# Kernel tuning notes

Hardware: AMD Instinct MI355X
Metric: run time of the kernel (lower is better)

Reference implementation:

```python
import jax, jax.numpy as jnp
import numpy as np

B, S, DIM, H, DH, DEPTH, NCLS = 4, 2048, 128, 8, 128, 2, 10
M = 128          # number of FAVOR+ random features
CHUNK = 128      # chunk size for causal linear attention
INNER = H * DH   # performer-pytorch: dim_head=dim -> inner_dim = heads*dim
FF = 4 * DIM


def layernorm(x, g, b, eps=1e-5):
    mu = jnp.mean(x, axis=-1, keepdims=True)
    var = jnp.mean((x - mu) ** 2, axis=-1, keepdims=True)
    return (x - mu) * jax.lax.rsqrt(var + eps) * g + b


def softmax_kernel(data, proj, is_query, eps=1e-4):
    # FAVOR+ positive softmax-kernel features. data: [B,H,S,DH], proj: [M,DH]
    norm = DH ** -0.25
    ratio = M ** -0.5
    d = data * norm
    dd = jnp.einsum('bhsd,md->bhsm', d, proj)
    diag = 0.5 * jnp.sum(d * d, axis=-1, keepdims=True)
    if is_query:
        stab = jnp.max(dd, axis=-1, keepdims=True)
    else:
        stab = jnp.max(dd, axis=(-2, -1), keepdims=True)
    stab = jax.lax.stop_gradient(stab)
    return ratio * (jnp.exp(dd - diag - stab) + eps)


def causal_linear_attention(qp, kp, v):
    # qp,kp: [B,H,S,M], v: [B,H,S,DH]; chunked prefix-sum causal linear attention
    b, h, s, m = qp.shape
    d = v.shape[-1]
    nc = s // CHUNK
    def to_chunks(t):
        return t.reshape(b, h, nc, CHUNK, -1).transpose(2, 0, 1, 3, 4)
    qc, kc, vc = to_chunks(qp), to_chunks(kp), to_chunks(v)
    tri = jnp.tril(jnp.ones((CHUNK, CHUNK), qp.dtype))
    def step(carry, inp):
        kv_sum, k_sum = carry           # [b,h,m,d], [b,h,m]
        qi, ki, vi = inp                # [b,h,CHUNK,*]
        attn = jnp.einsum('bhim,bhjm->bhij', qi, ki) * tri
        num = jnp.einsum('bhij,bhjd->bhid', attn, vi) \
            + jnp.einsum('bhim,bhmd->bhid', qi, kv_sum)
        den = jnp.sum(attn, axis=-1) + jnp.einsum('bhim,bhm->bhi', qi, k_sum)
        out = num / (den[..., None] + 1e-6)
        kv_sum = kv_sum + jnp.einsum('bhjm,bhjd->bhmd', ki, vi)
        k_sum = k_sum + jnp.sum(ki, axis=2)
        return (kv_sum, k_sum), out
    init = (jnp.zeros((b, h, m, d), qp.dtype), jnp.zeros((b, h, m), qp.dtype))
    _, out = jax.lax.scan(step, init, (qc, kc, vc))
    return out.transpose(1, 2, 0, 3, 4).reshape(b, h, s, d)


def setup_inputs():
    key = jax.random.key(0)
    ks = jax.random.split(key, 12)
    rng = np.random.default_rng(0)
    # sinusoidal positional encoding [S, DIM]
    pe = np.zeros((S, DIM), np.float32)
    pos = np.arange(S)[:, None].astype(np.float32)
    div = np.exp(np.arange(0, DIM, 2).astype(np.float32) * (-np.log(10000.0) / DIM))
    pe[:, 0::2] = np.sin(pos * div)
    pe[:, 1::2] = np.cos(pos * div)
    # orthogonal random feature projections per layer [DEPTH, M, DH]
    proj = np.stack([
        (np.linalg.qr(rng.standard_normal((DH, DH)))[0][:M] * np.sqrt(DH))
        for _ in range(DEPTH)
    ]).astype(np.float32)
    def gn(k, shape, scale):
        return jax.random.normal(k, shape, jnp.float32) * scale
    return {
        'x': gn(ks[0], (B, S, 1), 1.0),
        'lin_w': gn(ks[1], (1, DIM), 1.0),
        'lin_b': jnp.zeros((DIM,), jnp.float32),
        'pe': jnp.asarray(pe),
        'proj': jnp.asarray(proj),
        'ln1_g': jnp.ones((DEPTH, DIM), jnp.float32),
        'ln1_b': jnp.zeros((DEPTH, DIM), jnp.float32),
        'wq': gn(ks[2], (DEPTH, DIM, INNER), DIM ** -0.5),
        'wk': gn(ks[3], (DEPTH, DIM, INNER), DIM ** -0.5),
        'wv': gn(ks[4], (DEPTH, DIM, INNER), DIM ** -0.5),
        'wo': gn(ks[5], (DEPTH, INNER, DIM), INNER ** -0.5),
        'wo_b': jnp.zeros((DEPTH, DIM), jnp.float32),
        'ln2_g': jnp.ones((DEPTH, DIM), jnp.float32),
        'ln2_b': jnp.zeros((DEPTH, DIM), jnp.float32),
        'ff1_w': gn(ks[6], (DEPTH, DIM, FF), DIM ** -0.5),
        'ff1_b': jnp.zeros((DEPTH, FF), jnp.float32),
        'ff2_w': gn(ks[7], (DEPTH, FF, DIM), FF ** -0.5),
        'ff2_b': jnp.zeros((DEPTH, DIM), jnp.float32),
        'fin_w': gn(ks[8], (DIM, NCLS), DIM ** -0.5),
        'fin_b': jnp.zeros((NCLS,), jnp.float32),
    }


def reference(x, lin_w, lin_b, pe, proj, ln1_g, ln1_b, wq, wk, wv, wo, wo_b,
              ln2_g, ln2_b, ff1_w, ff1_b, ff2_w, ff2_b, fin_w, fin_b):
    h = x @ lin_w + lin_b            # [B,S,DIM]
    h = h + pe[None]
    for l in range(DEPTH):
        # --- pre-norm FAVOR+ causal self-attention ---
        y = layernorm(h, ln1_g[l], ln1_b[l])
        def split(t):  # [B,S,INNER] -> [B,H,S,DH]
            return t.reshape(B, S, H, DH).transpose(0, 2, 1, 3)
        q, k, v = split(y @ wq[l]), split(y @ wk[l]), split(y @ wv[l])
        qp = softmax_kernel(q, proj[l], True)
        kp = softmax_kernel(k, proj[l], False)
        o = causal_linear_attention(qp, kp, v)          # [B,H,S,DH]
        o = o.transpose(0, 2, 1, 3).reshape(B, S, INNER)
        h = h + (o @ wo[l] + wo_b[l])
        # --- pre-norm FFN ---
        y = layernorm(h, ln2_g[l], ln2_b[l])
        f = jax.nn.gelu(y @ ff1_w[l] + ff1_b[l]) @ ff2_w[l] + ff2_b[l]
        h = h + f
    pooled = jnp.mean(h, axis=1)     # [B,DIM]
    return pooled @ fin_w + fin_b    # [B,NCLS]
```

## Files before the change

kernel.cpp:

```cpp
#include <hip/hip_runtime.h>
#include <hip/hip_bf16.h>

#define Bb 4
#define Ss 2048
#define DIMc 128
#define Hh 8
#define DHc 128
#define Mf 128
#define CH 128
#define NCc 16
#define INNERc 1024
#define FFc 512

union F4 { float4 v; float f[4]; };
typedef unsigned short u16;

typedef __bf16 bf16x8 __attribute__((ext_vector_type(8)));
typedef float  f32x4  __attribute__((ext_vector_type(4)));

__device__ __forceinline__ unsigned fkey(float f){
  unsigned b = __float_as_uint(f);
  return (b & 0x80000000u) ? ~b : (b | 0x80000000u);
}
__device__ __forceinline__ float funkey(unsigned u){
  unsigned b = (u & 0x80000000u) ? (u & 0x7fffffffu) : ~u;
  return __uint_as_float(b);
}
__device__ __forceinline__ float gelu_f(float x){
  return 0.5f*x*(1.0f + tanhf(0.7978845608028654f*(x + 0.044715f*x*x*x)));
}
__device__ __forceinline__ u16 f2bu(float f){
  unsigned u = __float_as_uint(f);
  return (u16)((u + 0x7fffu + ((u>>16)&1u)) >> 16);
}
__device__ __forceinline__ float b2f(u16 u){
  return __uint_as_float(((unsigned)u)<<16);
}

__device__ __forceinline__ bf16x8 ldfrag(const u16* base, int row, int e){
  int byte = (row*256 + e*2) ^ ((row&7)<<4);
  return *(const bf16x8*)((const char*)base + byte);
}
__device__ __forceinline__ void stage_lin_bf(u16* dst, const u16* src, int srs, int t){
  #pragma unroll
  for(int it=0; it<8; ++it){
    int idx = t + it*256; int r = idx>>4, c8 = idx&15;
    int byte = (r*256 + c8*16) ^ ((r&7)<<4);
    *(uint4*)((char*)dst + byte) = *(const uint4*)(src + r*srs + c8*8);
  }
}
__device__ __forceinline__ void stage_lin_bf_s(u16* dst, const u16* src, int srs,
    int t, float sc, float off){
  #pragma unroll
  for(int it=0; it<8; ++it){
    int idx = t + it*256; int r = idx>>4, c8 = idx&15;
    u16 tmp[8]; *(uint4*)tmp = *(const uint4*)(src + r*srs + c8*8);
    #pragma unroll
    for(int u=0;u<8;u++) tmp[u] = f2bu(fmaf(b2f(tmp[u]), sc, off));
    int byte = (r*256 + c8*16) ^ ((r&7)<<4);
    *(uint4*)((char*)dst + byte) = *(uint4*)tmp;
  }
}
__device__ __forceinline__ void stage_lin_f32(u16* dst, const float* src, int srs, int t){
  #pragma unroll
  for(int it=0; it<8; ++it){
    int idx = t + it*256; int r = idx>>4, c8 = idx&15;
    F4 v0, v1;
    v0.v = *(const float4*)(src + r*srs + c8*8);
    v1.v = *(const float4*)(src + r*srs + c8*8 + 4);
    u16 tmp[8];
    #pragma unroll
    for(int u=0;u<4;u++){ tmp[u] = f2bu(v0.f[u]); tmp[4+u] = f2bu(v1.f[u]); }
    int byte = (r*256 + c8*16) ^ ((r&7)<<4);
    *(uint4*)((char*)dst + byte) = *(uint4*)tmp;
  }
}
__device__ __forceinline__ void stage_tr_bf(u16* dst, const u16* src, int srs, int t){
  int j0 = (t & 63)*2; int wv = t>>6;
  #pragma unroll
  for(int it=0; it<2; ++it){
    int d0 = wv*16 + it*64;
    u16 a0[16], a1[16];
    *(uint4*)&a0[0] = *(const uint4*)(src + j0*srs + d0);
    *(uint4*)&a0[8] = *(const uint4*)(src + j0*srs + d0 + 8);
    *(uint4*)&a1[0] = *(const uint4*)(src + (j0+1)*srs + d0);
    *(uint4*)&a1[8] = *(const uint4*)(src + (j0+1)*srs + d0 + 8);
    #pragma unroll
    for(int dc=0; dc<16; ++dc){
      int d = d0 + dc;
      unsigned pk = (unsigned)a0[dc] | ((unsigned)a1[dc]<<16);
      int byte = (d*256 + j0*2) ^ ((d&7)<<4);
      *(unsigned*)((char*)dst + byte) = pk;
    }
  }
}
__device__ __forceinline__ void stage_tr_bf_s(u16* dst, const u16* src, int srs,
    int t, float sc, float off){
  int j0 = (t & 63)*2; int wv = t>>6;
  #pragma unroll
  for(int it=0; it<2; ++it){
    int d0 = wv*16 + it*64;
    u16 a0[16], a1[16];
    *(uint4*)&a0[0] = *(const uint4*)(src + j0*srs + d0);
    *(uint4*)&a0[8] = *(const uint4*)(src + j0*srs + d0 + 8);
    *(uint4*)&a1[0] = *(const uint4*)(src + (j0+1)*srs + d0);
    *(uint4*)&a1[8] = *(const uint4*)(src + (j0+1)*srs + d0 + 8);
    #pragma unroll
    for(int dc=0; dc<16; ++dc){
      int d = d0 + dc;
      unsigned pk = (unsigned)f2bu(fmaf(b2f(a0[dc]), sc, off)) |
                    ((unsigned)f2bu(fmaf(b2f(a1[dc]), sc, off))<<16);
      int byte = (d*256 + j0*2) ^ ((d&7)<<4);
      *(unsigned*)((char*)dst + byte) = pk;
    }
  }
}

__device__ __forceinline__ int2 swz_tile(){
  int nx = gridDim.x;
  int nwg = gridDim.x*gridDim.y;
  int lin = blockIdx.y*nx + blockIdx.x;
  int q = nwg>>3, r = nwg&7;
  int xcd = lin&7, idx = lin>>3;
  int nl = (xcd<r) ? (xcd*(q+1)+idx) : (r*(q+1)+(xcd-r)*q+idx);
  return make_int2(nl % nx, nl / nx);
}

__global__ __launch_bounds__(64) void k_init(unsigned* kstab){
  if(threadIdx.x < 64) kstab[threadIdx.x] = 0u;
}

__global__ __launch_bounds__(256) void k_embed(const float* __restrict__ x,
    const float* __restrict__ lw, const float* __restrict__ lb,
    const float* __restrict__ pe, float* __restrict__ h){
  int idx = blockIdx.x*256 + threadIdx.x;
  int d = idx & 127; int bs = idx >> 7; int s = bs & (Ss-1);
  h[idx] = x[bs]*lw[d] + lb[d] + pe[s*DIMc + d];
}

__global__ __launch_bounds__(256) void k_ln(const float* __restrict__ in,
    const float* __restrict__ g, const float* __restrict__ bta,
    u16* __restrict__ out){
  int wave = threadIdx.x >> 6; int lane = threadIdx.x & 63;
  int row = blockIdx.x*4 + wave;
  const float* r = in + row*DIMc;
  float x1 = r[lane], x2 = r[lane+64];
  float s = x1+x2, sq = x1*x1 + x2*x2;
  #pragma unroll
  for(int m=1;m<64;m<<=1){ s += __shfl_xor(s,m,64); sq += __shfl_xor(sq,m,64); }
  float mu = s * (1.0f/128.0f);
  float var = sq*(1.0f/128.0f) - mu*mu;
  float rs = rsqrtf(var + 1e-5f);
  out[row*DIMc+lane]    = f2bu((x1-mu)*rs*g[lane]+bta[lane]);
  out[row*DIMc+lane+64] = f2bu((x2-mu)*rs*g[lane+64]+bta[lane+64]);
}

template<bool QKV3, bool BIAS, bool GELU>
__global__ __launch_bounds__(256) void k_gemm128(const u16* __restrict__ A,
    const float* __restrict__ B0, const float* __restrict__ B1,
    const float* __restrict__ B2, const float* __restrict__ bias,
    u16* __restrict__ C0, u16* __restrict__ C1, u16* __restrict__ C2,
    int N){
  __shared__ __align__(16) u16 As[16384];
  __shared__ __align__(16) u16 Bs[16384];
  int2 tt = swz_tile();
  int tn = tt.x, m0 = tt.y*128;
  const float* Bw; u16* C; int n0;
  if(QKV3){
    int tpw = N>>7;
    int widx = tn / tpw; n0 = (tn % tpw)*128;
    Bw = (widx==0) ? B0 : ((widx==1) ? B1 : B2);
    C  = (widx==0) ? C0 : ((widx==1) ? C1 : C2);
  } else { Bw = B0; C = C0; n0 = tn*128; }
  int t = threadIdx.x; int lane = t&63, w = t>>6;
  int fr = lane&15, kc = lane>>4;
  stage_lin_bf(As, A + (size_t)m0*128, 128, t);
  {
    #pragma unroll
    for(int it=0; it<8; ++it){
      int idx = t + it*256; int n = idx&127, c8 = idx>>7;
      u16 tmp[8];
      #pragma unroll
      for(int j=0;j<8;j++) tmp[j] = f2bu(Bw[(c8*8+j)*N + n0 + n]);
      int byte = (n*256 + c8*16) ^ ((n&7)<<4);
      *(uint4*)((char*)Bs + byte) = *(uint4*)tmp;
    }
  }
  __syncthreads();
  f32x4 acc[2][8] = {};
  #pragma unroll
  for(int ks=0; ks<4; ++ks){
    bf16x8 a[2];
    #pragma unroll
    for(int i=0;i<2;i++) a[i] = ldfrag(As, w*32+i*16+fr, ks*32+kc*8);
    bf16x8 bm[8];
    #pragma unroll
    for(int cb=0;cb<8;cb++) bm[cb] = ldfrag(Bs, cb*16+fr, ks*32+kc*8);
    #pragma unroll
    for(int i=0;i<2;i++)
      #pragma unroll
      for(int cb=0;cb<8;cb++)
        acc[i][cb] = __builtin_amdgcn_mfma_f32_16x16x32_bf16(a[i], bm[cb], acc[i][cb], 0,0,0);
  }
  #pragma unroll
  for(int i=0;i<2;i++){
    #pragma unroll
    for(int r=0;r<4;r++){
      int row = m0 + w*32 + i*16 + kc*4 + r;
      #pragma unroll
      for(int cb=0;cb<8;cb++){
        int col = n0 + cb*16 + fr;
        float val = acc[i][cb][r];
        if(BIAS) val += bias[col];
        if(GELU) val = gelu_f(val);
        C[(size_t)row*N + col] = f2bu(val);
      }
    }
  }
}

template<bool BIAS, bool GELU, bool RES, bool OBF>
__global__ __launch_bounds__(256) void k_gemm_bf(const u16* __restrict__ A,
    const float* __restrict__ Bw, const float* __restrict__ bias,
    const float* __restrict__ resid, void* __restrict__ Cp, int N, int K){
  __shared__ u16 As[64][40];
  __shared__ u16 Bs[64][40];
  int2 tt = swz_tile();
  int n0 = tt.x*64, m0 = tt.y*64;
  int t = threadIdx.x; int wid = t>>6, lane = t&63;
  int wr = wid>>1, wc = wid&1;
  int fr = lane&15, kc = lane>>4;
  f32x4 acc[2][2] = {};
  for(int k0=0; k0<K; k0+=32){
    {
      int r = t>>2, c8 = t&3;
      *(uint4*)&As[r][c8*8] = *(const uint4*)(A + (m0+r)*K + k0 + c8*8);
    }
    {
      int n = t&63, c8 = t>>6;
      u16 tmp[8];
      #pragma unroll
      for(int j=0;j<8;j++) tmp[j] = f2bu(Bw[(k0 + c8*8 + j)*N + n0 + n]);
      *(uint4*)&Bs[n][c8*8] = *(uint4*)tmp;
    }
    __syncthreads();
    bf16x8 af[2], bf[2];
    #pragma unroll
    for(int i=0;i<2;i++) af[i] = *(const bf16x8*)&As[wr*32 + i*16 + fr][kc*8];
    #pragma unroll
    for(int j=0;j<2;j++) bf[j] = *(const bf16x8*)&Bs[wc*32 + j*16 + fr][kc*8];
    #pragma unroll
    for(int i=0;i<2;i++)
      #pragma unroll
      for(int j=0;j<2;j++)
        acc[i][j] = __builtin_amdgcn_mfma_f32_16x16x32_bf16(af[i], bf[j], acc[i][j], 0, 0, 0);
    __syncthreads();
  }
  #pragma unroll
  for(int i=0;i<2;i++){
    #pragma unroll
    for(int r=0;r<4;r++){
      int row = m0 + wr*32 + i*16 + kc*4 + r;
      #pragma unroll
      for(int j=0;j<2;j++){
        int col = n0 + wc*32 + j*16 + fr;
        float val = acc[i][j][r];
        if(BIAS) val += bias[col];
        if(GELU) val = gelu_f(val);
        if(RES)  val += resid[row*N+col];
        if(OBF) ((u16*)Cp)[row*N+col] = f2bu(val);
        else    ((float*)Cp)[row*N+col] = val;
      }
    }
  }
}

template<bool ISQ>
__global__ __launch_bounds__(256) void k_featm(
    const u16* xin, u16* qout, const float* __restrict__ proj, unsigned* kstab){
  __shared__ __align__(16) u16 xs[16384];
  __shared__ __align__(16) u16 ps[16384];
  __shared__ float diag_s[128];
  __shared__ unsigned hmax[8];
  int r0 = blockIdx.x*128;
  int t = threadIdx.x; int lane = t&63, w = t>>6;
  int fr = lane&15, kc = lane>>4;
  const float norm  = 0.29730177875068026f;
  const float ratio = 0.08838834764831845f;
  if(!ISQ && t<8) hmax[t] = 0u;
  stage_lin_bf(xs, xin + (size_t)r0*128, 128, t);
  stage_lin_f32(ps, proj, 128, t);
  {
    int r = t>>1, half = t&1;
    const u16* rp = xin + (size_t)(r0+r)*128 + half*64;
    float ss = 0.f;
    #pragma unroll
    for(int u4=0; u4<8; ++u4){
      u16 tmp[8]; *(uint4*)tmp = *(const uint4*)(rp + u4*8);
      #pragma unroll
      for(int u=0;u<8;u++){ float f = b2f(tmp[u]); ss += f*f; }
    }
    ss += __shfl_xor(ss, 1, 64);
    if(half==0) diag_s[r] = 0.5f*norm*norm*ss;
  }
  __syncthreads();
  f32x4 acc[2][8] = {};
  #pragma unroll
  for(int ks=0; ks<4; ++ks){
    bf16x8 a[2];
    #pragma unroll
    for(int i=0;i<2;i++) a[i] = ldfrag(xs, w*32+i*16+fr, ks*32+kc*8);
    bf16x8 bm[8];
    #pragma unroll
    for(int cb=0;cb<8;cb++) bm[cb] = ldfrag(ps, cb*16+fr, ks*32+kc*8);
    #pragma unroll
    for(int i=0;i<2;i++)
      #pragma unroll
      for(int cb=0;cb<8;cb++)
        acc[i][cb] = __builtin_amdgcn_mfma_f32_16x16x32_bf16(a[i], bm[cb], acc[i][cb], 0,0,0);
  }
  __syncthreads();
  #pragma unroll
  for(int i=0;i<2;i++){
    #pragma unroll
    for(int r=0;r<4;r++){
      int row = w*32 + i*16 + kc*4 + r;
      float dg = diag_s[row];
      float rmax = acc[i][0][r];
      #pragma unroll
      for(int cb=1;cb<8;cb++) rmax = fmaxf(rmax, acc[i][cb][r]);
      #pragma unroll
      for(int msk=1;msk<16;msk<<=1) rmax = fmaxf(rmax, __shfl_xor(rmax, msk, 64));
      if(ISQ){
        float base = -dg - norm*rmax;
        #pragma unroll
        for(int cb=0;cb<8;cb++){
          float val = ratio*(expf(fmaf(norm, acc[i][cb][r], base)) + 1e-4f);
          int byte = (row*256 + (cb*16+fr)*2) ^ ((row&7)<<4);
          *(u16*)((char*)xs + byte) = f2bu(val);
        }
      } else {
        if(fr==0) atomicMax(&hmax[row&7], fkey(norm*rmax));
        #pragma unroll
        for(int cb=0;cb<8;cb++){
          float val = expf(fmaf(norm, acc[i][cb][r], -dg));
          int byte = (row*256 + (cb*16+fr)*2) ^ ((row&7)<<4);
          *(u16*)((char*)xs + byte) = f2bu(val);
        }
      }
    }
  }
  __syncthreads();
  #pragma unroll
  for(int it=0; it<8; ++it){
    int idx = t + it*256; int r = idx>>4, c8 = idx&15;
    int byte = (r*256 + c8*16) ^ ((r&7)<<4);
    *(uint4*)(qout + (size_t)(r0+r)*128 + c8*8) = *(uint4*)((char*)xs + byte);
  }
  if(!ISQ){
    int b = r0 >> 14;
    if(t<8) atomicMax(&kstab[b*8 + t], hmax[t]);
  }
}

__global__ __launch_bounds__(256) void k_attn1m(const u16* __restrict__ kp,
    const u16* __restrict__ v, u16* __restrict__ kvc, float* __restrict__ ksc,
    const unsigned* __restrict__ kstab){
  __shared__ __align__(16) u16 kt[16384];
  __shared__ __align__(16) u16 vt[16384];
  int bc = blockIdx.x; int c = bc&15, bh = bc>>4, b = bh>>3, hh = bh&7;
  int t = threadIdx.x; int lane = t&63, w = t>>6;
  int fr = lane&15, kc = lane>>4;
  int s0 = c*128;
  const float ratio = 0.08838834764831845f;
  float stab = funkey(kstab[bh]);
  float csc = ratio * expf(-stab);
  float reps = ratio * 1e-4f;
  const u16* kb = kp + (size_t)((b*Ss+s0)*Hh + hh)*128;
  const u16* vb = v  + (size_t)((b*Ss+s0)*Hh + hh)*128;
  stage_tr_bf_s(kt, kb, 1024, t, csc, reps);
  stage_tr_bf(vt, vb, 1024, t);
  __syncthreads();
  f32x4 acc[2][8] = {};
  f32x4 ks[2] = {};
  bf16x8 bones;
  #pragma unroll
  for(int e=0;e<8;e++) bones[e] = (fr==0) ? (__bf16)1.0f : (__bf16)0.0f;
  #pragma unroll
  for(int js=0;js<4;js++){
    bf16x8 am[2];
    #pragma unroll
    for(int i=0;i<2;i++) am[i] = ldfrag(kt, w*32+i*16+fr, js*32+kc*8);
    bf16x8 bv[8];
    #pragma unroll
    for(int cb=0;cb<8;cb++) bv[cb] = ldfrag(vt, cb*16+fr, js*32+kc*8);
    #pragma unroll
    for(int i=0;i<2;i++){
      ks[i] = __builtin_amdgcn_mfma_f32_16x16x32_bf16(am[i], bones, ks[i], 0,0,0);
      #pragma unroll
      for(int cb=0;cb<8;cb++)
        acc[i][cb] = __builtin_amdgcn_mfma_f32_16x16x32_bf16(am[i], bv[cb], acc[i][cb], 0,0,0);
    }
  }
  u16* kvb = kvc + (size_t)bc*16384;
  #pragma unroll
  for(int i=0;i<2;i++){
    #pragma unroll
    for(int r=0;r<4;r++){
      int m = w*32 + i*16 + kc*4 + r;
      #pragma unroll
      for(int cb=0;cb<8;cb++) kvb[m*128 + cb*16 + fr] = f2bu(acc[i][cb][r]);
      if(fr==0) ksc[bc*128 + m] = ks[i][r];
    }
  }
}

__global__ __launch_bounds__(256) void k_prefix2(unsigned* __restrict__ kvc,
    float* __restrict__ ksc){
  int blk = blockIdx.x;
  if(blk < 1024){
    int bh = blk >> 5; int pos = (blk & 31)*256 + threadIdx.x;
    int base = bh*16*8192 + pos;
    float a0 = 0.f, a1 = 0.f;
    #pragma unroll
    for(int c=0;c<16;c++){
      unsigned pk = kvc[base + c*8192];
      float x0 = b2f((u16)pk), x1 = b2f((u16)(pk>>16));
      kvc[base + c*8192] = (unsigned)f2bu(a0) | ((unsigned)f2bu(a1)<<16);
      a0 += x0; a1 += x1;
    }
  } else {
    int e = (blk-1024)*256 + threadIdx.x;
    int bh = e>>7, m = e&127;
    float a = 0.f;
    #pragma unroll
    for(int c=0;c<16;c++){
      int idx = (bh*16+c)*128 + m;
      float xv = ksc[idx]; ksc[idx] = a; a += xv;
    }
  }
}

__global__ __launch_bounds__(256) void k_attn2m(const u16* __restrict__ qp,
    const u16* __restrict__ kp, const u16* __restrict__ v,
    const u16* __restrict__ kvc, const float* __restrict__ ksc,
    u16* __restrict__ o, const unsigned* __restrict__ kstab){
  __shared__ __align__(16) u16 qs[16384];
  __shared__ __align__(16) u16 bs[16384];
  __shared__ float ksum_s[128];
  int bc = blockIdx.x; int c = bc&15, bh = bc>>4, b = bh>>3, hh = bh&7;
  int t = threadIdx.x; int lane = t&63, w = t>>6;
  int fr = lane&15, kc = lane>>4;
  int s0 = c*128;
  const float ratio = 0.08838834764831845f;
  float stab = funkey(kstab[bh]);
  float csc = ratio * expf(-stab);
  float reps = ratio * 1e-4f;
  const u16* qb = qp + (size_t)((b*Ss+s0)*Hh + hh)*128;
  const u16* kb = kp + (size_t)((b*Ss+s0)*Hh + hh)*128;
  const u16* vb = v  + (size_t)((b*Ss+s0)*Hh + hh)*128;
  const u16* kvb = kvc + (size_t)bc*16384;
  stage_lin_bf(qs, qb, 1024, t);
  stage_lin_bf_s(bs, kb, 1024, t, csc, reps);
  if(t<128) ksum_s[t] = ksc[bc*128 + t];
  __syncthreads();
  bf16x8 aq[2][4];
  #pragma unroll
  for(int i=0;i<2;i++)
    #pragma unroll
    for(int ks=0;ks<4;ks++)
      aq[i][ks] = ldfrag(qs, w*32+i*16+fr, ks*32+kc*8);
  f32x4 sacc[2][8] = {};
  #pragma unroll
  for(int ks=0;ks<4;ks++){
    bf16x8 bk[8];
    #pragma unroll
    for(int cb=0;cb<8;cb++) bk[cb] = ldfrag(bs, cb*16+fr, ks*32+kc*8);
    #pragma unroll
    for(int i=0;i<2;i++)
      #pragma unroll
      for(int cb=0;cb<8;cb++)
        sacc[i][cb] = __builtin_amdgcn_mfma_f32_16x16x32_bf16(aq[i][ks], bk[cb], sacc[i][cb], 0,0,0);
  }
  __syncthreads();
  #pragma unroll
  for(int i=0;i<2;i++){
    #pragma unroll
    for(int cb=0;cb<8;cb++){
      #pragma unroll
      for(int r=0;r<4;r++){
        int prow = w*32 + i*16 + kc*4 + r;
        int pcol = cb*16 + fr;
        float pv = (pcol > prow) ? 0.f : sacc[i][cb][r];
        int byte = (prow*256 + pcol*2) ^ ((prow&7)<<4);
        *(u16*)((char*)qs + byte) = f2bu(pv);
      }
    }
  }
  stage_tr_bf(bs, vb, 1024, t);
  __syncthreads();
  f32x4 nacc[2][8] = {};
  f32x4 dacc[2] = {};
  bf16x8 bones;
  #pragma unroll
  for(int e=0;e<8;e++) bones[e] = (fr==0) ? (__bf16)1.0f : (__bf16)0.0f;
  #pragma unroll
  for(int js=0;js<4;js++){
    bf16x8 ap[2];
    #pragma unroll
    for(int i=0;i<2;i++) ap[i] = ldfrag(qs, w*32+i*16+fr, js*32+kc*8);
    bf16x8 bv[8];
    #pragma unroll
    for(int cb=0;cb<8;cb++) bv[cb] = ldfrag(bs, cb*16+fr, js*32+kc*8);
    #pragma unroll
    for(int i=0;i<2;i++){
      dacc[i] = __builtin_amdgcn_mfma_f32_16x16x32_bf16(ap[i], bones, dacc[i], 0,0,0);
      #pragma unroll
      for(int cb=0;cb<8;cb++)
        nacc[i][cb] = __builtin_amdgcn_mfma_f32_16x16x32_bf16(ap[i], bv[cb], nacc[i][cb], 0,0,0);
    }
  }
  __syncthreads();
  stage_tr_bf(bs, kvb, 128, t);
  __syncthreads();
  #pragma unroll
  for(int ms=0;ms<4;ms++){
    bf16x8 bkv[8];
    #pragma unroll
    for(int cb=0;cb<8;cb++) bkv[cb] = ldfrag(bs, cb*16+fr, ms*32+kc*8);
    bf16x8 bks;
    #pragma unroll
    for(int e=0;e<8;e++) bks[e] = (fr==0) ? (__bf16)ksum_s[ms*32+kc*8+e] : (__bf16)0.0f;
    #pragma unroll
    for(int i=0;i<2;i++){
      dacc[i] = __builtin_amdgcn_mfma_f32_16x16x32_bf16(aq[i][ms], bks, dacc[i], 0,0,0);
      #pragma unroll
      for(int cb=0;cb<8;cb++)
        nacc[i][cb] = __builtin_amdgcn_mfma_f32_16x16x32_bf16(aq[i][ms], bkv[cb], nacc[i][cb], 0,0,0);
    }
  }
  #pragma unroll
  for(int i=0;i<2;i++){
    #pragma unroll
    for(int r=0;r<4;r++){
      float den = __shfl(dacc[i][r], lane & 48, 64);
      float inv = 1.0f/(den + 1e-6f);
      int row = w*32 + i*16 + kc*4 + r;
      u16* ob = o + (size_t)((b*Ss+s0+row)*Hh + hh)*128;
      #pragma unroll
      for(int cb=0;cb<8;cb++)
        ob[cb*16 + fr] = f2bu(nacc[i][cb][r] * inv);
    }
  }
}

__global__ __launch_bounds__(256) void k_pool(const float* __restrict__ h,
    float* __restrict__ pw){
  __shared__ float part[256];
  int blk = blockIdx.x; int b = blk>>4, c = blk&15;
  int t = threadIdx.x; int half = t>>7;
  float s = 0.f;
  int s0 = c*128 + half*64;
  for(int si=s0; si<s0+64; ++si) s += h[(b*Ss+si)*128 + (t&127)];
  part[t] = s;
  __syncthreads();
  if(t<128) pw[blk*128 + t] = part[t] + part[t+128];
}
__global__ __launch_bounds__(128) void k_cls(const float* __restrict__ pw,
    const float* __restrict__ fw, const float* __restrict__ fb,
    float* __restrict__ out){
  __shared__ float pool_s[128];
  int b = blockIdx.x; int t = threadIdx.x;
  float s = 0.f;
  for(int c=0;c<16;c++) s += pw[(b*16+c)*128 + t];
  pool_s[t] = s * (1.0f/2048.0f);
  __syncthreads();
  if(t<10){
    float a = fb[t];
    for(int d=0; d<128; ++d) a += pool_s[d]*fw[d*10+t];
    out[b*10+t] = a;
  }
}

extern "C" void kernel_launch(void* const* d_in, const int* in_sizes, int n_in,
                              void* d_out, int out_size, void* d_ws, size_t ws_size,
                              hipStream_t stream){
  (void)in_sizes; (void)n_in; (void)out_size; (void)ws_size;
  const float* x     = (const float*)d_in[0];
  const float* lin_w = (const float*)d_in[1];
  const float* lin_b = (const float*)d_in[2];
  const float* pe    = (const float*)d_in[3];
  const float* proj  = (const float*)d_in[4];
  const float* ln1_g = (const float*)d_in[5];
  const float* ln1_b = (const float*)d_in[6];
  const float* wq    = (const float*)d_in[7];
  const float* wk    = (const float*)d_in[8];
  const float* wv    = (const float*)d_in[9];
  const float* wo    = (const float*)d_in[10];
  const float* wo_b  = (const float*)d_in[11];
  const float* ln2_g = (const float*)d_in[12];
  const float* ln2_b = (const float*)d_in[13];
  const float* ff1w  = (const float*)d_in[14];
  const float* ff1b  = (const float*)d_in[15];
  const float* ff2w  = (const float*)d_in[16];
  const float* ff2b  = (const float*)d_in[17];
  const float* finw  = (const float*)d_in[18];
  const float* finb  = (const float*)d_in[19];
  float* out = (float*)d_out;

  float* ws  = (float*)d_ws;
  float* h    = ws;
  u16*  y    = (u16*)(h + 1048576);
  u16*  q    = (u16*)(h + 1048576 + 524288);
  u16*  k    = q + 8388608;
  u16*  v    = k + 8388608;
  u16*  o    = v + 8388608;
  u16*  kvc  = o + 8388608;
  float* ksc  = (float*)(kvc + 8388608);
  float* pw   = ksc + 65536;
  unsigned* kstab = (unsigned*)(pw + 8192);

  k_init<<<1,64,0,stream>>>(kstab);
  k_embed<<<4096,256,0,stream>>>(x, lin_w, lin_b, pe, h);
  for(int l=0;l<2;l++){
    const float* projl = proj + l*Mf*DHc;
    k_ln<<<2048,256,0,stream>>>(h, ln1_g + l*DIMc, ln1_b + l*DIMc, y);
    k_gemm128<true,false,false><<<dim3(24,64),256,0,stream>>>(
        y, wq + l*DIMc*INNERc, wk + l*DIMc*INNERc, wv + l*DIMc*INNERc,
        nullptr, q, k, v, INNERc);
    k_featm<true><<<512,256,0,stream>>>(q, q, projl, nullptr);
    k_featm<false><<<512,256,0,stream>>>(k, k, projl, kstab + l*32);
    k_attn1m<<<512,256,0,stream>>>(k, v, kvc, ksc, kstab + l*32);
    k_prefix2<<<1040,256,0,stream>>>((unsigned*)kvc, ksc);
    k_attn2m<<<512,256,0,stream>>>(q, k, v, kvc, ksc, o, kstab + l*32);
    k_gemm_bf<true,false,true,false><<<dim3(2,128),256,0,stream>>>(o, wo + l*INNERc*DIMc, wo_b + l*DIMc, h, h, DIMc, INNERc);
    k_ln<<<2048,256,0,stream>>>(h, ln2_g + l*DIMc, ln2_b + l*DIMc, y);
    k_gemm128<false,true,true><<<dim3(4,64),256,0,stream>>>(
        y, ff1w + l*DIMc*FFc, nullptr, nullptr, ff1b + l*FFc,
        q, nullptr, nullptr, FFc);
    k_gemm_bf<true,false,true,false><<<dim3(2,128),256,0,stream>>>(q, ff2w + l*FFc*DIMc, ff2b + l*DIMc, h, h, DIMc, FFc);
  }
  k_pool<<<64,256,0,stream>>>(h, pw);
  k_cls<<<4,128,0,stream>>>(pw, finw, finb, out);
}
```

Measured before the change: 438.1 us.

## Fuse QKV projection with FAVOR+ feature map into single kernel

The QKV GEMM kernel now computes the FAVOR+ random-feature projection, diagonal term, row max and exp for Q and K tiles straight from its fp32 accumulators, and writes the features directly. The two separate feature-map kernels, with their global round trip of q and k, go away. The diagonal is computed from fp32 accumulators rather than rounded bf16 values. The fused kernel does more shared-memory work per block and uses more registers, which may reduce occupancy.

Measured after the change: 454.4 us. 1.04x slower.

```diff
diff --git a/kernel.cpp b/kernel.cpp
--- a/kernel.cpp
+++ b/kernel.cpp
@@ -155,23 +155,152 @@
   out[row*DIMc+lane+64] = f2bu((x2-mu)*rs*g[lane+64]+bta[lane+64]);
 }
 
-template<bool QKV3, bool BIAS, bool GELU>
+__global__ __launch_bounds__(256) void k_qkvf(const u16* __restrict__ y,
+    const float* __restrict__ wq, const float* __restrict__ wk,
+    const float* __restrict__ wv, const float* __restrict__ proj,
+    u16* __restrict__ q, u16* __restrict__ k, u16* __restrict__ v,
+    unsigned* __restrict__ kstab){
+  __shared__ __align__(16) u16 As[16384];
+  __shared__ __align__(16) u16 Bs[16384];
+  __shared__ unsigned hmax_s;
+  int2 tt = swz_tile();
+  int tn = tt.x, m0 = tt.y*128;
+  int widx = tn>>3, hh = tn&7, n0 = hh*128;
+  const float* Bw = (widx==0) ? wq : ((widx==1) ? wk : wv);
+  int t = threadIdx.x; int lane = t&63, w = t>>6;
+  int fr = lane&15, kc = lane>>4;
+  const float norm  = 0.29730177875068026f;
+  const float ratio = 0.08838834764831845f;
+  if(t==0) hmax_s = 0u;
+  stage_lin_bf(As, y + (size_t)m0*128, 128, t);
+  {
+    #pragma unroll
+    for(int it=0; it<8; ++it){
+      int idx = t + it*256; int n = idx&127, c8 = idx>>7;
+      u16 tmp[8];
+      #pragma unroll
+      for(int j=0;j<8;j++) tmp[j] = f2bu(Bw[(c8*8+j)*INNERc + n0 + n]);
+      int byte = (n*256 + c8*16) ^ ((n&7)<<4);
+      *(uint4*)((char*)Bs + byte) = *(uint4*)tmp;
+    }
+  }
+  __syncthreads();
+  f32x4 acc[2][8] = {};
+  #pragma unroll
+  for(int ks=0; ks<4; ++ks){
+    bf16x8 a[2];
+    #pragma unroll
+    for(int i=0;i<2;i++) a[i] = ldfrag(As, w*32+i*16+fr, ks*32+kc*8);
+    bf16x8 bm[8];
+    #pragma unroll
+    for(int cb=0;cb<8;cb++) bm[cb] = ldfrag(Bs, cb*16+fr, ks*32+kc*8);
+    #pragma unroll
+    for(int i=0;i<2;i++)
+      #pragma unroll
+      for(int cb=0;cb<8;cb++)
+        acc[i][cb] = __builtin_amdgcn_mfma_f32_16x16x32_bf16(a[i], bm[cb], acc[i][cb], 0,0,0);
+  }
+  if(widx==2){
+    #pragma unroll
+    for(int i=0;i<2;i++)
+      #pragma unroll
+      for(int r=0;r<4;r++){
+        int row = m0 + w*32 + i*16 + kc*4 + r;
+        #pragma unroll
+        for(int cb=0;cb<8;cb++)
+          v[(size_t)row*INNERc + n0 + cb*16 + fr] = f2bu(acc[i][cb][r]);
+      }
+    return;
+  }
+  float dg[2][4];
+  #pragma unroll
+  for(int i=0;i<2;i++)
+    #pragma unroll
+    for(int r=0;r<4;r++){
+      float s = 0.f;
+      #pragma unroll
+      for(int cb=0;cb<8;cb++){ float fv = acc[i][cb][r]; s += fv*fv; }
+      #pragma unroll
+      for(int msk=1;msk<16;msk<<=1) s += __shfl_xor(s, msk, 64);
+      dg[i][r] = 0.5f*norm*norm*s;
+    }
+  __syncthreads();
+  #pragma unroll
+  for(int i=0;i<2;i++)
+    #pragma unroll
+    for(int cb=0;cb<8;cb++)
+      #pragma unroll
+      for(int r=0;r<4;r++){
+        int prow = w*32 + i*16 + kc*4 + r;
+        int pcol = cb*16 + fr;
+        int byte = (prow*256 + pcol*2) ^ ((prow&7)<<4);
+        *(u16*)((char*)As + byte) = f2bu(acc[i][cb][r]);
+      }
+  stage_lin_f32(Bs, proj, 128, t);
+  __syncthreads();
+  f32x4 dacc[2][8] = {};
+  #pragma unroll
+  for(int ks=0; ks<4; ++ks){
+    bf16x8 a[2];
+    #pragma unroll
+    for(int i=0;i<2;i++) a[i] = ldfrag(As, w*32+i*16+fr, ks*32+kc*8);
+    bf16x8 bm[8];
+    #pragma unroll
+    for(int cb=0;cb<8;cb++) bm[cb] = ldfrag(Bs, cb*16+fr, ks*32+kc*8);
+    #pragma unroll
+    for(int i=0;i<2;i++)
+      #pragma unroll
+      for(int cb=0;cb<8;cb++)
+        dacc[i][cb] = __builtin_amdgcn_mfma_f32_16x16x32_bf16(a[i], bm[cb], dacc[i][cb], 0,0,0);
+  }
+  __syncthreads();
+  #pragma unroll
+  for(int i=0;i<2;i++)
+    #pragma unroll
+    for(int r=0;r<4;r++){
+      int prow = w*32 + i*16 + kc*4 + r;
+      float rmax = dacc[i][0][r];
+      #pragma unroll
+      for(int cb=1;cb<8;cb++) rmax = fmaxf(rmax, dacc[i][cb][r]);
+      #pragma unroll
+      for(int msk=1;msk<16;msk<<=1) rmax = fmaxf(rmax, __shfl_xor(rmax, msk, 64));
+      if(widx==0){
+        float base = -dg[i][r] - norm*rmax;
+        #pragma unroll
+        for(int cb=0;cb<8;cb++){
+          float val = ratio*(expf(fmaf(norm, dacc[i][cb][r], base)) + 1e-4f);
+          int byte = (prow*256 + (cb*16+fr)*2) ^ ((prow&7)<<4);
+          *(u16*)((char*)As + byte) = f2bu(val);
+        }
+      } else {
+        if(fr==0) atomicMax(&hmax_s, fkey(norm*rmax));
+        #pragma unroll
+        for(int cb=0;cb<8;cb++){
+          float val = expf(fmaf(norm, dacc[i][cb][r], -dg[i][r]));
+          int byte = (prow*256 + (cb*16+fr)*2) ^ ((prow&7)<<4);
+          *(u16*)((char*)As + byte) = f2bu(val);
+        }
+      }
+    }
+  __syncthreads();
+  u16* outp = (widx==0) ? q : k;
+  #pragma unroll
+  for(int it=0; it<8; ++it){
+    int idx = t + it*256; int r = idx>>4, c8 = idx&15;
+    int byte = (r*256 + c8*16) ^ ((r&7)<<4);
+    *(uint4*)(outp + (size_t)(m0+r)*INNERc + n0 + c8*8) = *(uint4*)((char*)As + byte);
+  }
+  if(widx==1 && t==0) atomicMax(&kstab[(m0>>11)*8 + hh], hmax_s);
+}
+
+template<bool BIAS, bool GELU>
 __global__ __launch_bounds__(256) void k_gemm128(const u16* __restrict__ A,
-    const float* __restrict__ B0, const float* __restrict__ B1,
-    const float* __restrict__ B2, const float* __restrict__ bias,
-    u16* __restrict__ C0, u16* __restrict__ C1, u16* __restrict__ C2,
-    int N){
+    const float* __restrict__ B0, const float* __restrict__ bias,
+    u16* __restrict__ C0, int N){
   __shared__ __align__(16) u16 As[16384];
   __shared__ __align__(16) u16 Bs[16384];
   int2 tt = swz_tile();
-  int tn = tt.x, m0 = tt.y*128;
-  const float* Bw; u16* C; int n0;
-  if(QKV3){
-    int tpw = N>>7;
-    int widx = tn / tpw; n0 = (tn % tpw)*128;
-    Bw = (widx==0) ? B0 : ((widx==1) ? B1 : B2);
-    C  = (widx==0) ? C0 : ((widx==1) ? C1 : C2);
-  } else { Bw = B0; C = C0; n0 = tn*128; }
+  int n0 = tt.x*128, m0 = tt.y*128;
   int t = threadIdx.x; int lane = t&63, w = t>>6;
   int fr = lane&15, kc = lane>>4;
   stage_lin_bf(As, A + (size_t)m0*128, 128, t);
@@ -181,7 +310,7 @@
       int idx = t + it*256; int n = idx&127, c8 = idx>>7;
       u16 tmp[8];
       #pragma unroll
-      for(int j=0;j<8;j++) tmp[j] = f2bu(Bw[(c8*8+j)*N + n0 + n]);
+      for(int j=0;j<8;j++) tmp[j] = f2bu(B0[(c8*8+j)*N + n0 + n]);
       int byte = (n*256 + c8*16) ^ ((n&7)<<4);
       *(uint4*)((char*)Bs + byte) = *(uint4*)tmp;
     }
@@ -213,7 +342,7 @@
         float val = acc[i][cb][r];
         if(BIAS) val += bias[col];
         if(GELU) val = gelu_f(val);
-        C[(size_t)row*N + col] = f2bu(val);
+        C0[(size_t)row*N + col] = f2bu(val);
       }
     }
   }
@@ -272,94 +401,6 @@
         else    ((float*)Cp)[row*N+col] = val;
       }
     }
-  }
-}
-
-template<bool ISQ>
-__global__ __launch_bounds__(256) void k_featm(
-    const u16* xin, u16* qout, const float* __restrict__ proj, unsigned* kstab){
-  __shared__ __align__(16) u16 xs[16384];
-  __shared__ __align__(16) u16 ps[16384];
-  __shared__ float diag_s[128];
-  __shared__ unsigned hmax[8];
-  int r0 = blockIdx.x*128;
-  int t = threadIdx.x; int lane = t&63, w = t>>6;
-  int fr = lane&15, kc = lane>>4;
-  const float norm  = 0.29730177875068026f;
-  const float ratio = 0.08838834764831845f;
-  if(!ISQ && t<8) hmax[t] = 0u;
-  stage_lin_bf(xs, xin + (size_t)r0*128, 128, t);
-  stage_lin_f32(ps, proj, 128, t);
-  {
-    int r = t>>1, half = t&1;
-    const u16* rp = xin + (size_t)(r0+r)*128 + half*64;
-    float ss = 0.f;
-    #pragma unroll
-    for(int u4=0; u4<8; ++u4){
-      u16 tmp[8]; *(uint4*)tmp = *(const uint4*)(rp + u4*8);
-      #pragma unroll
-      for(int u=0;u<8;u++){ float f = b2f(tmp[u]); ss += f*f; }
-    }
-    ss += __shfl_xor(ss, 1, 64);
-    if(half==0) diag_s[r] = 0.5f*norm*norm*ss;
-  }
-  __syncthreads();
-  f32x4 acc[2][8] = {};
-  #pragma unroll
-  for(int ks=0; ks<4; ++ks){
-    bf16x8 a[2];
-    #pragma unroll
-    for(int i=0;i<2;i++) a[i] = ldfrag(xs, w*32+i*16+fr, ks*32+kc*8);
-    bf16x8 bm[8];
-    #pragma unroll
-    for(int cb=0;cb<8;cb++) bm[cb] = ldfrag(ps, cb*16+fr, ks*32+kc*8);
-    #pragma unroll
-    for(int i=0;i<2;i++)
-      #pragma unroll
-      for(int cb=0;cb<8;cb++)
-        acc[i][cb] = __builtin_amdgcn_mfma_f32_16x16x32_bf16(a[i], bm[cb], acc[i][cb], 0,0,0);
-  }
-  __syncthreads();
-  #pragma unroll
-  for(int i=0;i<2;i++){
-    #pragma unroll
-    for(int r=0;r<4;r++){
-      int row = w*32 + i*16 + kc*4 + r;
-      float dg = diag_s[row];
-      float rmax = acc[i][0][r];
-      #pragma unroll
-      for(int cb=1;cb<8;cb++) rmax = fmaxf(rmax, acc[i][cb][r]);
-      #pragma unroll
-      for(int msk=1;msk<16;msk<<=1) rmax = fmaxf(rmax, __shfl_xor(rmax, msk, 64));
-      if(ISQ){
-        float base = -dg - norm*rmax;
-        #pragma unroll
-        for(int cb=0;cb<8;cb++){
-          float val = ratio*(expf(fmaf(norm, acc[i][cb][r], base)) + 1e-4f);
-          int byte = (row*256 + (cb*16+fr)*2) ^ ((row&7)<<4);
-          *(u16*)((char*)xs + byte) = f2bu(val);
-        }
-      } else {
-        if(fr==0) atomicMax(&hmax[row&7], fkey(norm*rmax));
-        #pragma unroll
-        for(int cb=0;cb<8;cb++){
-          float val = expf(fmaf(norm, acc[i][cb][r], -dg));
-          int byte = (row*256 + (cb*16+fr)*2) ^ ((row&7)<<4);
-          *(u16*)((char*)xs + byte) = f2bu(val);
-        }
-      }
-    }
-  }
-  __syncthreads();
-  #pragma unroll
-  for(int it=0; it<8; ++it){
-    int idx = t + it*256; int r = idx>>4, c8 = idx&15;
-    int byte = (r*256 + c8*16) ^ ((r&7)<<4);
-    *(uint4*)(qout + (size_t)(r0+r)*128 + c8*8) = *(uint4*)((char*)xs + byte);
-  }
-  if(!ISQ){
-    int b = r0 >> 14;
-    if(t<8) atomicMax(&kstab[b*8 + t], hmax[t]);
   }
 }
 
@@ -625,19 +666,16 @@
   for(int l=0;l<2;l++){
     const float* projl = proj + l*Mf*DHc;
     k_ln<<<2048,256,0,stream>>>(h, ln1_g + l*DIMc, ln1_b + l*DIMc, y);
-    k_gemm128<true,false,false><<<dim3(24,64),256,0,stream>>>(
+    k_qkvf<<<dim3(24,64),256,0,stream>>>(
         y, wq + l*DIMc*INNERc, wk + l*DIMc*INNERc, wv + l*DIMc*INNERc,
-        nullptr, q, k, v, INNERc);
-    k_featm<true><<<512,256,0,stream>>>(q, q, projl, nullptr);
-    k_featm<false><<<512,256,0,stream>>>(k, k, projl, kstab + l*32);
+        projl, q, k, v, kstab + l*32);
     k_attn1m<<<512,256,0,stream>>>(k, v, kvc, ksc, kstab + l*32);
     k_prefix2<<<1040,256,0,stream>>>((unsigned*)kvc, ksc);
     k_attn2m<<<512,256,0,stream>>>(q, k, v, kvc, ksc, o, kstab + l*32);
     k_gemm_bf<true,false,true,false><<<dim3(2,128),256,0,stream>>>(o, wo + l*INNERc*DIMc, wo_b + l*DIMc, h, h, DIMc, INNERc);
     k_ln<<<2048,256,0,stream>>>(h, ln2_g + l*DIMc, ln2_b + l*DIMc, y);
-    k_gemm128<false,true,true><<<dim3(4,64),256,0,stream>>>(
-        y, ff1w + l*DIMc*FFc, nullptr, nullptr, ff1b + l*FFc,
-        q, nullptr, nullptr, FFc);
+    k_gemm128<true,true><<<dim3(4,64),256,0,stream>>>(
+        y, ff1w + l*DIMc*FFc, ff1b + l*FFc, q, FFc);
     k_gemm_bf<true,false,true,false><<<dim3(2,128),256,0,stream>>>(q, ff2w + l*FFc*DIMc, ff2b + l*DIMc, h, h, DIMc, FFc);
   }
   k_pool<<<64,256,0,stream>>>(h, pw);
```
